# Kernel optimization log

Hardware: AMD Instinct MI355X
Metric: run time of the kernel (lower is better)

Reference implementation:

```python
import jax, jax.numpy as jnp
import numpy as np

BS = 256          # batch_size
NN = BS - 1
D = 128           # projection dim
SIGMA = 0.07      # rbf gamma (self.sigma)
C = 1.0
REG = 0.1
NUM_ITERS = 1000
ETA = 0.001
USE_NORM = True


def setup_inputs() -> dict:
    key = jax.random.key(0)
    k1, k2 = jax.random.split(key)
    z = jax.random.normal(k1, (BS, 2, D), dtype=jnp.float32)
    alpha_init = jax.random.normal(k2, (BS, NN, 1), dtype=jnp.float32)
    return {"z": z, "alpha_init": alpha_init}


def _rbf_kernel(X, Y, gamma):
    # exp(-gamma * ||x - y||^2)
    xn = jnp.sum(X * X, axis=1, keepdims=True)          # [n,1]
    yn = jnp.sum(Y * Y, axis=1, keepdims=True).T        # [1,m]
    d = xn + yn - 2.0 * (X @ Y.T)
    return jnp.exp(-gamma * d)


def _pgd_nesterov(DD, p, alpha0, eta, num_iters, C, use_norm):
    # minimize 0.5 a'DDa - p'a  s.t. 0 <= a <= C, batched over bs
    def step(carry, t):
        alpha, alpha_prev = carry
        beta = t / (t + 3.0)
        y = alpha + beta * (alpha - alpha_prev)
        grad = jnp.einsum('bij,bjk->bik', DD, y) - p     # [bs,nn,1]
        if use_norm:
            grad = grad / (jnp.linalg.norm(grad, axis=1, keepdims=True) + 1e-12)
        alpha_new = jnp.clip(y - eta * grad, 0.0, C)
        return (alpha_new, alpha), None
    (alpha, _), _ = jax.lax.scan(step, (alpha0, alpha0),
                                 jnp.arange(num_iters, dtype=jnp.float32))
    return alpha


def reference(z, alpha_init):
    bs, nn = BS, NN
    # F.normalize(z, p=2, dim=1): normalize over the view axis (faithful to source)
    nrm = jnp.maximum(jnp.linalg.norm(z, axis=1, keepdims=True), 1e-12)
    ftr = z / nrm
    ftr = jnp.concatenate([ftr[:, 0, :], ftr[:, 1, :]], axis=0)   # [2bs, d]

    K = _rbf_kernel(ftr[:bs], ftr, SIGMA)                          # [bs, 2bs]

    # ---- QP construction + solve under no_grad ----
    Kd = jax.lax.stop_gradient(K)
    KK = Kd[:, :bs]                                                # block: first bs cols
    r = jnp.arange(bs)
    m = jnp.arange(nn)
    # idx[i] = [0..bs-1] without i  (KMASK row/col removal)
    idx = m[None, :] + (m[None, :] >= r[:, None]).astype(jnp.int32)  # [bs, nn]
    KK_sub = KK[idx[:, :, None], idx[:, None, :]]                  # [bs,nn,nn]
    row = jnp.take_along_axis(KK, idx, axis=1)                     # row[i,m]=KK[i,idx[i,m]]
    # Delta[i,j,k] = 1 + reg*d_jk + KK[j,k] - KK[i,j] - KK[i,k]  (j,k != i)
    DD = (1.0 + REG * jnp.eye(nn, dtype=KK.dtype)[None]
          + KK_sub - row[:, :, None] - row[:, None, :])            # [bs,nn,nn]

    p = 2.0 * jnp.ones((bs, nn, 1), dtype=jnp.float32)
    alpha0 = jnp.clip(jax.nn.relu(alpha_init), 0.0, C)
    alpha = _pgd_nesterov(DD, p, alpha0, ETA, NUM_ITERS, C, USE_NORM)
    alpha_y = jnp.clip(jax.nn.relu(alpha[:, :, 0]), 0.0, C)
    alpha_y = jax.lax.stop_gradient(alpha_y)                       # [bs,nn]
    alpha_x = alpha_y.sum(axis=1)                                  # [bs]

    # ---- loss terms (grad flows through K here) ----
    Ks = K[:, bs:]                                                 # block12: [bs,bs]
    # Kn.T[i,m] = Ks.T[i, idx[i,m]]  (neg_mask = off-diagonal)
    KnT = jnp.take_along_axis(Ks.T, idx, axis=1)                   # [bs,nn]
    pos = jnp.diagonal(Ks)                                         # pos_mask = eye
    pos_loss = jnp.mean(alpha_x * pos)
    neg_loss = jnp.sum(alpha_y * KnT) / bs
    loss = neg_loss - pos_loss

    sparsity = ((alpha_y == C).sum().astype(jnp.float32)
                / ((alpha_y > 0).sum().astype(jnp.float32) + 1e-10))
    num_zero = (alpha_y == 0.0).mean()
    return (loss, pos.mean(), KnT.mean(), sparsity, num_zero, jnp.float32(0.0))
```

## Files before the change

kernel.cpp:

```cpp
#include <hip/hip_runtime.h>
#include <math.h>

#define BS   256
#define NN   255
#define DIM  128
#define GAMMA 0.07
#define NUM_ITERS 1000

typedef float v2f __attribute__((ext_vector_type(2)));

__device__ __forceinline__ double wred_d(double v) {
  #pragma unroll
  for (int k = 1; k < 64; k <<= 1) v += __shfl_xor(v, k, 64);
  return v;
}
__device__ __forceinline__ int wred_i(int v) {
  #pragma unroll
  for (int k = 1; k < 64; k <<= 1) v += __shfl_xor(v, k, 64);
  return v;
}

__device__ __forceinline__ float RLF(float v, int lane) {
  return __int_as_float(__builtin_amdgcn_readlane(__float_as_int(v), lane));
}

template <int CTRL, int RMASK>
__device__ __forceinline__ float dpp_add(float x) {
  int t = __builtin_amdgcn_update_dpp(0, __float_as_int(x), CTRL, RMASK, 0xf, true);
  return x + __int_as_float(t);
}
__device__ __forceinline__ float wred64_dpp(float x) {
  x = dpp_add<0x111, 0xf>(x);
  x = dpp_add<0x112, 0xf>(x);
  x = dpp_add<0x114, 0xf>(x);
  x = dpp_add<0x118, 0xf>(x);
  x = dpp_add<0x142, 0xa>(x);
  x = dpp_add<0x143, 0xc>(x);
  return RLF(x, 63);
}

__device__ __forceinline__ float rsq_nr(float x) {
  float r;
  asm("v_rsq_f32 %0, %1" : "=v"(r) : "v"(x));
  r = r * (1.5f - 0.5f * x * r * r);
  return r;
}

__device__ __forceinline__ void pk_fma(v2f& acc, const v2f& k, const v2f& y) {
  asm("v_pk_fma_f32 %0, %1, %2, %0" : "+v"(acc) : "v"(k), "v"(y));
}

__device__ __forceinline__ float4 add4(float4 a, float4 b) {
  float4 c; c.x = a.x + b.x; c.y = a.y + b.y; c.z = a.z + b.z; c.w = a.w + b.w;
  return c;
}

__global__ void k_ftr(const float* __restrict__ z, double* __restrict__ ftrT) {
  int b = blockIdx.x;
  int d = threadIdx.x;
  double z0 = (double)z[b * 256 + d];
  double z1 = (double)z[b * 256 + 128 + d];
  double n = sqrt(z0 * z0 + z1 * z1);
  n = fmax(n, 1e-12);
  ftrT[d * 512 + b]       = z0 / n;
  ftrT[d * 512 + 256 + b] = z1 / n;
}

__global__ void k_K(const double* __restrict__ ftrT, float* __restrict__ K,
                    double* __restrict__ pk_knt, double* __restrict__ pos_arr) {
  int i = blockIdx.x;
  int t = threadIdx.x;
  __shared__ double rowi[DIM];
  __shared__ double redd[4];
  if (t < DIM) rowi[t] = ftrT[t * 512 + i];
  __syncthreads();
  double xn = 0.0;
  #pragma unroll 8
  for (int d = 0; d < DIM; ++d) xn += rowi[d] * rowi[d];

  double knt_part = 0.0;
  #pragma unroll
  for (int h = 0; h < 2; ++h) {
    int j = t + h * 256;
    double dot = 0.0, sq = 0.0;
    #pragma unroll 8
    for (int d = 0; d < DIM; ++d) {
      double f = ftrT[d * 512 + j];
      dot += rowi[d] * f;
      sq  += f * f;
    }
    double dist = xn + sq - 2.0 * dot;
    double kv = exp(-GAMMA * dist);
    K[i * 512 + j] = (float)kv;
    if (h == 1) {
      if (j == 256 + i) pos_arr[i] = kv;
      else knt_part += kv;
    }
  }
  double w = wred_d(knt_part);
  if ((t & 63) == 0) redd[t >> 6] = w;
  __syncthreads();
  if (t == 0) pk_knt[i] = redd[0] + redd[1] + redd[2] + redd[3];
}

__global__ __launch_bounds__(512, 2) void k_pgd(
    const float* __restrict__ K, const float* __restrict__ alpha_init,
    double* __restrict__ neg_arr, double* __restrict__ sa_arr,
    int* __restrict__ cnt1, int* __restrict__ cntp, int* __restrict__ cnt0) {
  int r = blockIdx.x;
  int tid = threadIdx.x;
  int l = tid & 63;
  int rg = tid >> 6;

  __shared__ __align__(16) float part[2][8][BS];
  __shared__ __align__(16) float ywave[8][32];
  __shared__ float betat[1024];

  for (int i = tid; i < 1024; i += 512)
    betat[i] = (float)i / ((float)i + 3.0f);

  v2f kq[64];
  #pragma unroll
  for (int j = 0; j < 16; ++j) {
    float4 r0 = *(const float4*)&K[(32 * rg + 2 * j + 0) * 512 + 4 * l];
    float4 r1 = *(const float4*)&K[(32 * rg + 2 * j + 1) * 512 + 4 * l];
    kq[j].x      = r0.x; kq[j].y      = r1.x;
    kq[16 + j].x = r0.y; kq[16 + j].y = r1.y;
    kq[32 + j].x = r0.z; kq[32 + j].y = r1.z;
    kq[48 + j].x = r0.w; kq[48 + j].y = r1.w;
  }
  #pragma unroll
  for (int j = 0; j < 64; ++j)
    asm volatile("" : "+v"(kq[j]));

  float al[4], ap[4], yv[4], kv[4], rm2[4];
  #pragma unroll
  for (int k = 0; k < 4; ++k) {
    int a = 4 * l + k;
    if (a == r) {
      al[k] = 0.f; ap[k] = 0.f; yv[k] = 0.f; kv[k] = 0.f; rm2[k] = 0.f;
    } else {
      int c = a - (a > r ? 1 : 0);
      float v = alpha_init[r * NN + c];
      v = fminf(fmaxf(v, 0.f), 1.f);
      al[k] = v; ap[k] = v; yv[k] = v;
      kv[k] = 1.0f - K[r * 512 + a];
      rm2[k] = 2.0f;
    }
  }
  if ((l >> 3) == rg) {
    float4 y4 = {yv[0], yv[1], yv[2], yv[3]};
    *(float4*)&ywave[rg][4 * (l & 7)] = y4;
  }
  __syncthreads();

  int rq = r >> 2, rc = r & 3;

  for (int it = 0; it < NUM_ITERS; ++it) {
    float (*pb)[BS] = part[it & 1];

    const float4* yb = (const float4*)&ywave[rg][0];
    v2f a0 = {0.f, 0.f}, a1 = {0.f, 0.f}, a2 = {0.f, 0.f}, a3 = {0.f, 0.f};
    #pragma unroll
    for (int jj = 0; jj < 8; ++jj) {
      float4 yq = yb[jj];
      v2f ylo = {yq.x, yq.y};
      v2f yhi = {yq.z, yq.w};
      pk_fma(a0, kq[2 * jj],      ylo); pk_fma(a0, kq[2 * jj + 1],      yhi);
      pk_fma(a1, kq[16 + 2 * jj], ylo); pk_fma(a1, kq[16 + 2 * jj + 1], yhi);
      pk_fma(a2, kq[32 + 2 * jj], ylo); pk_fma(a2, kq[32 + 2 * jj + 1], yhi);
      pk_fma(a3, kq[48 + 2 * jj], ylo); pk_fma(a3, kq[48 + 2 * jj + 1], yhi);
    }
    float4 accw = {a0.x + a0.y, a1.x + a1.y, a2.x + a2.y, a3.x + a3.y};
    *(float4*)&pb[rg][4 * l] = accw;
    __syncthreads();

    float4 q0 = *(const float4*)&pb[0][4 * l];
    float4 q1 = *(const float4*)&pb[1][4 * l];
    float4 q2 = *(const float4*)&pb[2][4 * l];
    float4 q3 = *(const float4*)&pb[3][4 * l];
    float4 q4 = *(const float4*)&pb[4][4 * l];
    float4 q5 = *(const float4*)&pb[5][4 * l];
    float4 q6 = *(const float4*)&pb[6][4 * l];
    float4 q7 = *(const float4*)&pb[7][4 * l];
    float4 gA = add4(add4(add4(q0, q1), add4(q2, q3)),
                     add4(add4(q4, q5), add4(q6, q7)));
    float grv = (rc == 0) ? gA.x : (rc == 1) ? gA.y : (rc == 2) ? gA.z : gA.w;
    float gr = RLF(grv, rq);
    float Sv = wred64_dpp((yv[0] + yv[1]) + (yv[2] + yv[3]));
    float beta = betat[it + 1];
    float g[4];
    g[0] = (gA.x - gr) - rm2[0] + kv[0] * Sv + 0.1f * yv[0];
    g[1] = (gA.y - gr) - rm2[1] + kv[1] * Sv + 0.1f * yv[1];
    g[2] = (gA.z - gr) - rm2[2] + kv[2] * Sv + 0.1f * yv[2];
    g[3] = (gA.w - gr) - rm2[3] + kv[3] * Sv + 0.1f * yv[3];
    float n2 = wred64_dpp((g[0] * g[0] + g[1] * g[1]) + (g[2] * g[2] + g[3] * g[3]));
    float sinv = 0.001f * rsq_nr(n2);
    #pragma unroll
    for (int k = 0; k < 4; ++k) {
      float na = fminf(fmaxf(fmaf(-sinv, g[k], yv[k]), 0.f), 1.f);
      ap[k] = al[k];
      al[k] = na;
      yv[k] = fmaf(beta, na - ap[k], na);
    }
    if ((l >> 3) == rg) {
      float4 y4 = {yv[0], yv[1], yv[2], yv[3]};
      *(float4*)&ywave[rg][4 * (l & 7)] = y4;
    }
  }

  if (rg == 0) {
    double nl = 0.0, sa = 0.0;
    int c1 = 0, cp = 0, cz = 0;
    #pragma unroll
    for (int k = 0; k < 4; ++k) {
      int a = 4 * l + k;
      if (a != r) {
        float kx = K[a * 512 + 256 + r];
        nl += (double)al[k] * (double)kx;
        sa += (double)al[k];
        c1 += (al[k] == 1.0f);
        cp += (al[k] > 0.0f);
        cz += (al[k] == 0.0f);
      }
    }
    nl = wred_d(nl); sa = wred_d(sa);
    c1 = wred_i(c1); cp = wred_i(cp); cz = wred_i(cz);
    if (l == 0) {
      neg_arr[r] = nl;
      sa_arr[r]  = sa;
      cnt1[r] = c1; cntp[r] = cp; cnt0[r] = cz;
    }
  }
}

__global__ void k_fin(const double* __restrict__ pk_knt, const double* __restrict__ pos_arr,
                      const double* __restrict__ neg_arr, const double* __restrict__ sa_arr,
                      const int* __restrict__ cnt1, const int* __restrict__ cntp,
                      const int* __restrict__ cnt0, float* __restrict__ out) {
  int t = threadIdx.x;
  __shared__ double rd[16];
  __shared__ int ri[12];
  double knt = pk_knt[t];
  double pos = pos_arr[t];
  double neg = neg_arr[t];
  double pl  = sa_arr[t] * pos_arr[t];
  int a1 = cnt1[t], ap = cntp[t], a0 = cnt0[t];
  knt = wred_d(knt); pos = wred_d(pos); neg = wred_d(neg); pl = wred_d(pl);
  a1 = wred_i(a1); ap = wred_i(ap); a0 = wred_i(a0);
  int w = t >> 6;
  if ((t & 63) == 0) {
    rd[w] = knt; rd[4 + w] = pos; rd[8 + w] = neg; rd[12 + w] = pl;
    ri[w] = a1; ri[4 + w] = ap; ri[8 + w] = a0;
  }
  __syncthreads();
  if (t == 0) {
    double kntS = rd[0] + rd[1] + rd[2] + rd[3];
    double posS = rd[4] + rd[5] + rd[6] + rd[7];
    double negS = rd[8] + rd[9] + rd[10] + rd[11];
    double plS  = rd[12] + rd[13] + rd[14] + rd[15];
    int c1t = ri[0] + ri[1] + ri[2] + ri[3];
    int cpt = ri[4] + ri[5] + ri[6] + ri[7];
    int c0t = ri[8] + ri[9] + ri[10] + ri[11];
    out[0] = (float)(negS / 256.0 - plS / 256.0);
    out[1] = (float)(posS / 256.0);
    out[2] = (float)(kntS / (256.0 * 255.0));
    out[3] = (float)c1t / ((float)cpt + 1e-10f);
    out[4] = (float)c0t / 65280.0f;
    out[5] = 0.0f;
  }
}

extern "C" void kernel_launch(void* const* d_in, const int* in_sizes, int n_in,
                              void* d_out, int out_size, void* d_ws, size_t ws_size,
                              hipStream_t stream) {
  const float* z     = (const float*)d_in[0];
  const float* ainit = (const float*)d_in[1];
  char* ws = (char*)d_ws;
  double* ftrT   = (double*)ws;
  float*  K      = (float*)(ws + 524288);
  double* pk_knt = (double*)(ws + 1048576);
  double* pos_a  = (double*)(ws + 1048576 + 2048);
  double* neg_a  = (double*)(ws + 1048576 + 4096);
  double* sa_a   = (double*)(ws + 1048576 + 6144);
  int* cnt1 = (int*)(ws + 1048576 + 8192);
  int* cntp = (int*)(ws + 1048576 + 8192 + 1024);
  int* cnt0 = (int*)(ws + 1048576 + 8192 + 2048);
  float* out = (float*)d_out;

  k_ftr<<<256, 128, 0, stream>>>(z, ftrT);
  k_K  <<<256, 256, 0, stream>>>(ftrT, K, pk_knt, pos_a);
  k_pgd<<<256, 512, 0, stream>>>(K, ainit, neg_a, sa_a, cnt1, cntp, cnt0);
  k_fin<<<1, 256, 0, stream>>>(pk_knt, pos_a, neg_a, sa_a, cnt1, cntp, cnt0, out);
}
```

Baseline: 912.2 us.

## Repartition PGD matvec so waves own column blocks and reduce rows via shuffles

New measurement: 1.008 ms. 10.5% more time.

```diff
diff --git a/kernel.cpp b/kernel.cpp
--- a/kernel.cpp
+++ b/kernel.cpp
@@ -48,11 +48,6 @@
 
 __device__ __forceinline__ void pk_fma(v2f& acc, const v2f& k, const v2f& y) {
   asm("v_pk_fma_f32 %0, %1, %2, %0" : "+v"(acc) : "v"(k), "v"(y));
-}
-
-__device__ __forceinline__ float4 add4(float4 a, float4 b) {
-  float4 c; c.x = a.x + b.x; c.y = a.y + b.y; c.z = a.z + b.z; c.w = a.w + b.w;
-  return c;
 }
 
 __global__ void k_ftr(const float* __restrict__ z, double* __restrict__ ftrT) {
@@ -111,9 +106,11 @@
   int tid = threadIdx.x;
   int l = tid & 63;
   int rg = tid >> 6;
-
-  __shared__ __align__(16) float part[2][8][BS];
-  __shared__ __align__(16) float ywave[8][32];
+  int m = l >> 3;
+  int cb = 32 * rg + 4 * (l & 7);
+
+  __shared__ __align__(16) float ytil2[8 * 36];
+  __shared__ __align__(16) float gAshare[2][BS];
   __shared__ float betat[1024];
 
   for (int i = tid; i < 1024; i += 512)
@@ -122,8 +119,8 @@
   v2f kq[64];
   #pragma unroll
   for (int j = 0; j < 16; ++j) {
-    float4 r0 = *(const float4*)&K[(32 * rg + 2 * j + 0) * 512 + 4 * l];
-    float4 r1 = *(const float4*)&K[(32 * rg + 2 * j + 1) * 512 + 4 * l];
+    float4 r0 = *(const float4*)&K[(32 * m + 2 * j + 0) * 512 + cb];
+    float4 r1 = *(const float4*)&K[(32 * m + 2 * j + 1) * 512 + cb];
     kq[j].x      = r0.x; kq[j].y      = r1.x;
     kq[16 + j].x = r0.y; kq[16 + j].y = r1.y;
     kq[32 + j].x = r0.z; kq[32 + j].y = r1.z;
@@ -148,18 +145,18 @@
       rm2[k] = 2.0f;
     }
   }
-  if ((l >> 3) == rg) {
+  {
     float4 y4 = {yv[0], yv[1], yv[2], yv[3]};
-    *(float4*)&ywave[rg][4 * (l & 7)] = y4;
+    *(float4*)&ytil2[36 * (l >> 3) + ((4 * l) & 31)] = y4;
   }
   __syncthreads();
 
   int rq = r >> 2, rc = r & 3;
 
   for (int it = 0; it < NUM_ITERS; ++it) {
-    float (*pb)[BS] = part[it & 1];
-
-    const float4* yb = (const float4*)&ywave[rg][0];
+    float beta = betat[it + 1];
+
+    const float4* yb = (const float4*)&ytil2[36 * m];
     v2f a0 = {0.f, 0.f}, a1 = {0.f, 0.f}, a2 = {0.f, 0.f}, a3 = {0.f, 0.f};
     #pragma unroll
     for (int jj = 0; jj < 8; ++jj) {
@@ -172,23 +169,21 @@
       pk_fma(a3, kq[48 + 2 * jj], ylo); pk_fma(a3, kq[48 + 2 * jj + 1], yhi);
     }
     float4 accw = {a0.x + a0.y, a1.x + a1.y, a2.x + a2.y, a3.x + a3.y};
-    *(float4*)&pb[rg][4 * l] = accw;
+    #pragma unroll
+    for (int mask = 8; mask <= 32; mask <<= 1) {
+      accw.x += __shfl_xor(accw.x, mask, 64);
+      accw.y += __shfl_xor(accw.y, mask, 64);
+      accw.z += __shfl_xor(accw.z, mask, 64);
+      accw.w += __shfl_xor(accw.w, mask, 64);
+    }
+    if (l < 8) *(float4*)&gAshare[it & 1][32 * rg + 4 * l] = accw;
+
+    float Sv = wred64_dpp((yv[0] + yv[1]) + (yv[2] + yv[3]));
     __syncthreads();
 
-    float4 q0 = *(const float4*)&pb[0][4 * l];
-    float4 q1 = *(const float4*)&pb[1][4 * l];
-    float4 q2 = *(const float4*)&pb[2][4 * l];
-    float4 q3 = *(const float4*)&pb[3][4 * l];
-    float4 q4 = *(const float4*)&pb[4][4 * l];
-    float4 q5 = *(const float4*)&pb[5][4 * l];
-    float4 q6 = *(const float4*)&pb[6][4 * l];
-    float4 q7 = *(const float4*)&pb[7][4 * l];
-    float4 gA = add4(add4(add4(q0, q1), add4(q2, q3)),
-                     add4(add4(q4, q5), add4(q6, q7)));
+    float4 gA = *(const float4*)&gAshare[it & 1][4 * l];
     float grv = (rc == 0) ? gA.x : (rc == 1) ? gA.y : (rc == 2) ? gA.z : gA.w;
     float gr = RLF(grv, rq);
-    float Sv = wred64_dpp((yv[0] + yv[1]) + (yv[2] + yv[3]));
-    float beta = betat[it + 1];
     float g[4];
     g[0] = (gA.x - gr) - rm2[0] + kv[0] * Sv + 0.1f * yv[0];
     g[1] = (gA.y - gr) - rm2[1] + kv[1] * Sv + 0.1f * yv[1];
@@ -203,10 +198,8 @@
       al[k] = na;
       yv[k] = fmaf(beta, na - ap[k], na);
     }
-    if ((l >> 3) == rg) {
-      float4 y4 = {yv[0], yv[1], yv[2], yv[3]};
-      *(float4*)&ywave[rg][4 * (l & 7)] = y4;
-    }
+    float4 y4 = {yv[0], yv[1], yv[2], yv[3]};
+    *(float4*)&ytil2[36 * (l >> 3) + ((4 * l) & 31)] = y4;
   }
 
   if (rg == 0) {
```
